# Optimization experiments

Hardware: AMD Instinct MI355X
Metric: run time of the kernel (lower is better)

## Reference

```python
import jax, jax.numpy as jnp
import numpy as np

B, D = 8192, 512
MARGIN, CR_BETA, NUM_CLASSES = 0.2, 0.1, 1000


def setup_inputs() -> dict:
    key = jax.random.key(0)
    k1, k2, k3, k4 = jax.random.split(key, 4)
    return {
        "img": jax.random.normal(k1, (B, D), jnp.float32),
        "txt": jax.random.normal(k2, (B, D), jnp.float32),
        "txt_cr": jax.random.normal(k3, (B, D), jnp.float32),
        "labels": jax.random.randint(k4, (B,), 0, NUM_CLASSES),
        "auto_margin_flag": 1,
        "margin": jnp.full((B,), MARGIN, jnp.float32),  # opt.margin repeated per row
        "cr_beta": CR_BETA,
    }


def _similarity(a, b):
    # row-normalize then full cosine-similarity matrix + matched (diagonal) sims
    an = a / (jnp.linalg.norm(a, axis=1, keepdims=True) + 1e-8)
    bn = b / (jnp.linalg.norm(b, axis=1, keepdims=True) + 1e-8)
    return an @ bn.T, jnp.sum(an * bn, axis=1)


def _dir_loss(sim, labels, margin, auto_flag):
    # semi-hard negative mining per anchor row, fully vectorized.
    # Deterministic stand-in for np.random.choice: first valid negative index.
    diag = jnp.diagonal(sim)                               # sim[idx, idx]
    neg_mask = labels[None, :] != labels[:, None]          # [B,B] negatives
    loss_mat = sim - diag[:, None] + margin[:, None]       # triplet margin term
    valid = neg_mask & (loss_mat > 0) & (loss_mat < margin[:, None])
    valid = jax.lax.stop_gradient(valid)                   # mining is detached (numpy in torch)
    has_valid = jnp.any(valid, axis=1)
    if auto_flag:
        row_ok = (margin >= 0.16) & has_valid
    else:
        row_ok = has_valid
    neg_idx = jnp.argmax(valid, axis=1)                    # first valid negative
    sim_an = jnp.take_along_axis(sim, neg_idx[:, None], axis=1)[:, 0]
    per_row = jax.nn.relu(margin - diag + sim_an)
    return jnp.sum(jnp.where(row_ok, per_row, 0.0))


def _cr_loss(img, txt, txt_cr, labels, auto_flag, margin, cr_beta):
    sim, sm = _similarity(img, txt)
    sim_cr, sm_cr = _similarity(img, txt_cr)
    if auto_flag:
        lam = jnp.abs(jax.lax.stop_gradient(sm_cr)) / jnp.abs(jax.lax.stop_gradient(sm))
        lam = jnp.minimum(lam, 1.0)                        # clamp lambda_cr to <= 1
        margin_cr = (lam + 1.0) * margin / 2.0
    else:
        margin_cr = margin / 2.0
    margin_cr = jax.lax.stop_gradient(margin_cr)
    base = _dir_loss(sim, labels, margin, auto_flag) + _dir_loss(sim.T, labels, margin, auto_flag)
    cr = _dir_loss(sim_cr, labels, margin_cr, auto_flag) + _dir_loss(sim_cr.T, labels, margin_cr, auto_flag)
    return base + cr_beta * cr


def reference(img, txt, txt_cr, labels, auto_margin_flag, margin, cr_beta):
    return _cr_loss(img, txt, txt_cr, labels, bool(auto_margin_flag), margin, cr_beta)
```

## Files before the change

kernel.cpp:

```cpp
#include <hip/hip_runtime.h>
#include <climits>

#define NB 8192
#define ND 512

#define WCHUNKS 16
#define WMAXT 4
#define TCHUNKS ((NB - 64) / 64)


__global__ __launch_bounds__(256) void stats_k(
        const float* __restrict__ img, const float* __restrict__ txt,
        const float* __restrict__ cr, const float* __restrict__ margin,
        const int* __restrict__ flagp,
        float* rnImg, float* rnTxt, float* rnCr,
        float* dgSim, float* dgCr, float* mgCr,
        int* negIdx, int* stragCnt, float* out) {
    int tid = threadIdx.x, bid = blockIdx.x;
    int g = bid * 256 + tid;
    if (g < 4 * NB) negIdx[g] = INT_MAX;
    if (bid == 0 && tid < 8) stragCnt[tid] = 0;
    if (bid == 0 && tid == 0) out[0] = 0.0f;

    int r = bid * 16 + (tid >> 4);
    int q = tid & 15;
    const float4* iv = (const float4*)(img + (size_t)r * ND);
    const float4* tv = (const float4*)(txt + (size_t)r * ND);
    const float4* cv = (const float4*)(cr  + (size_t)r * ND);
    float sii = 0, stt = 0, scc = 0, sit = 0, sic = 0;
    #pragma unroll
    for (int i = 0; i < 8; ++i) {
        int k = q + i * 16;
        float4 x = iv[k], y = tv[k], w = cv[k];
        sii += x.x*x.x + x.y*x.y + x.z*x.z + x.w*x.w;
        stt += y.x*y.x + y.y*y.y + y.z*y.z + y.w*y.w;
        scc += w.x*w.x + w.y*w.y + w.z*w.z + w.w*w.w;
        sit += x.x*y.x + x.y*y.y + x.z*y.z + x.w*y.w;
        sic += x.x*w.x + x.y*w.y + x.z*w.z + x.w*w.w;
    }
    #pragma unroll
    for (int off = 1; off < 16; off <<= 1) {
        sii += __shfl_xor(sii, off); stt += __shfl_xor(stt, off);
        scc += __shfl_xor(scc, off); sit += __shfl_xor(sit, off);
        sic += __shfl_xor(sic, off);
    }
    if (q == 0) {
        float rnI = 1.0f / (sqrtf(sii) + 1e-8f);
        float rnT = 1.0f / (sqrtf(stt) + 1e-8f);
        float rnC = 1.0f / (sqrtf(scc) + 1e-8f);
        float ds = sit * rnI * rnT;
        float dc = sic * rnI * rnC;
        float m  = margin[r];
        float mcr = flagp[0] ? (fminf(fabsf(dc) / fabsf(ds), 1.0f) + 1.0f) * m * 0.5f
                             : m * 0.5f;
        rnImg[r] = rnI; rnTxt[r] = rnT; rnCr[r] = rnC;
        dgSim[r] = ds;  dgCr[r]  = dc;  mgCr[r] = mcr;
    }
}

__device__ inline void pass_arrays(int z,
        const float* img, const float* txt, const float* cr,
        const float* rnImg, const float* rnTxt, const float* rnCr,
        const float* dgSim, const float* dgCr,
        const float* margin, const float* mgCr,
        const float*& A, const float*& B, const float*& rnA, const float*& rnB,
        const float*& dgA, const float*& mgA) {
    if (z == 0)      { A = img; B = txt; rnA = rnImg; rnB = rnTxt; dgA = dgSim; mgA = margin; }
    else if (z == 1) { A = txt; B = img; rnA = rnTxt; rnB = rnImg; dgA = dgSim; mgA = margin; }
    else if (z == 2) { A = img; B = cr;  rnA = rnImg; rnB = rnCr;  dgA = dgCr;  mgA = mgCr;   }
    else             { A = cr;  B = img; rnA = rnCr;  rnB = rnImg; dgA = dgCr;  mgA = mgCr;   }
}

__global__ __launch_bounds__(256) void band_k(
        const float* __restrict__ img, const float* __restrict__ txt,
        const float* __restrict__ cr, const int* __restrict__ labels,
        const int* __restrict__ flagp, const float* __restrict__ margin,
        const float* __restrict__ betap,
        const float* rnImg, const float* rnTxt, const float* rnCr,
        const float* dgSim, const float* dgCr, const float* mgCr,
        int* stragCnt, int* stragList, float* out) {
    __shared__ __align__(16) float As[16][64];
    __shared__ __align__(16) float Bs[16][64];
    __shared__ float aRn[64], aDg[64], aMg[64], colRn[64];
    __shared__ int   aLab[64], colLab[64], resIdx[64];
    __shared__ float blockAcc;

    const int tid = threadIdx.x, z = blockIdx.y, a0 = blockIdx.x * 64;
    const int flag = flagp[0];
    const float *A, *B, *rnA, *rnB, *dgA, *mgA;
    pass_arrays(z, img, txt, cr, rnImg, rnTxt, rnCr, dgSim, dgCr, margin, mgCr,
                A, B, rnA, rnB, dgA, mgA);

    if (tid < 64) {
        int a = a0 + tid;
        float mg = mgA[a];
        aRn[tid] = rnA[a]; aDg[tid] = dgA[a]; aMg[tid] = mg;
        aLab[tid] = labels[a];
        colRn[tid] = rnB[tid]; colLab[tid] = labels[tid];
        resIdx[tid] = (flag && mg < 0.16f) ? -1 : INT_MAX;
    }
    if (tid == 0) blockAcc = 0.0f;

    const int ty4  = (tid >> 4) * 4, tx4 = (tid & 15) * 4;
    const int lrow = tid >> 2,  lk4 = (tid & 3) * 4;

    float acc[4][4];
    #pragma unroll
    for (int i = 0; i < 4; ++i)
        #pragma unroll
        for (int j = 0; j < 4; ++j) acc[i][j] = 0.0f;

    float4 va = *(const float4*)(A + (size_t)(a0 + lrow) * ND + lk4);
    float4 vb = *(const float4*)(B + (size_t)lrow * ND + lk4);
    for (int kc = 0; kc < ND; kc += 16) {
        __syncthreads();
        As[lk4 + 0][lrow] = va.x; As[lk4 + 1][lrow] = va.y;
        As[lk4 + 2][lrow] = va.z; As[lk4 + 3][lrow] = va.w;
        Bs[lk4 + 0][lrow] = vb.x; Bs[lk4 + 1][lrow] = vb.y;
        Bs[lk4 + 2][lrow] = vb.z; Bs[lk4 + 3][lrow] = vb.w;
        if (kc + 16 < ND) {
            va = *(const float4*)(A + (size_t)(a0 + lrow) * ND + kc + 16 + lk4);
            vb = *(const float4*)(B + (size_t)lrow * ND + kc + 16 + lk4);
        }
        __syncthreads();
        #pragma unroll
        for (int k = 0; k < 16; ++k) {
            float4 av = *(const float4*)&As[k][ty4];
            float4 bv = *(const float4*)&Bs[k][tx4];
            float ar[4] = {av.x, av.y, av.z, av.w};
            float br[4] = {bv.x, bv.y, bv.z, bv.w};
            #pragma unroll
            for (int i = 0; i < 4; ++i)
                #pragma unroll
                for (int j = 0; j < 4; ++j)
                    acc[i][j] = fmaf(ar[i], br[j], acc[i][j]);
        }
    }
    __syncthreads();

    #pragma unroll
    for (int i = 0; i < 4; ++i) {
        int r = ty4 + i;
        float mgv = aMg[r];
        if (flag && mgv < 0.16f) continue;
        float dg = aDg[r], rna = aRn[r];
        int la = aLab[r];
        #pragma unroll
        for (int j = 0; j < 4; ++j) {
            int c = tx4 + j;
            if (colLab[c] == la) continue;
            float v  = acc[i][j] * rna * colRn[c];
            float lm = v - dg + mgv;
            if (lm > 0.0f && lm < mgv) atomicMin(&resIdx[r], c);
        }
    }
    __syncthreads();

    #pragma unroll
    for (int i = 0; i < 4; ++i) {
        int r = ty4 + i;
        int w = resIdx[r];
        if (w < 0 || w == INT_MAX) continue;
        int c = w - tx4;
        if (c < 0 || c > 3) continue;
        float v  = acc[i][c] * aRn[r] * colRn[w];
        float lm = v - aDg[r] + aMg[r];
        atomicAdd(&blockAcc, lm);
    }
    __syncthreads();

    if (tid < 64 && resIdx[tid] == INT_MAX) {
        int pos = atomicAdd(&stragCnt[z], 1);
        stragList[z * NB + pos] = a0 + tid;
    }
    if (tid == 0 && blockAcc != 0.0f) {
        float scale = (z >= 2) ? betap[0] : 1.0f;
        atomicAdd(out, blockAcc * scale);
    }
}

__global__ __launch_bounds__(256) void wina_k(
        const float* __restrict__ img, const float* __restrict__ txt,
        const float* __restrict__ cr, const int* __restrict__ labels,
        const float* __restrict__ margin,
        const float* rnImg, const float* rnTxt, const float* rnCr,
        const float* dgSim, const float* dgCr, const float* mgCr,
        const int* stragCnt, const int* stragList, int* negIdx) {
    __shared__ __align__(16) float As[16][64];
    __shared__ __align__(16) float Bs[16][64];
    __shared__ float aRn[64], aDg[64], aMg[64], colRn[64];
    __shared__ int   aId[64], aRowS[64], aLab[64], colLab[64];

    const int tid = threadIdx.x, z = blockIdx.y;
    const int chunk = blockIdx.x & (WCHUNKS - 1);
    const int t     = blockIdx.x / WCHUNKS;
    const int cnt = stragCnt[z];
    if (t * 64 >= cnt) return;
    const int c0 = 64 + chunk * 64;

    const float *A, *B, *rnA, *rnB, *dgA, *mgA;
    pass_arrays(z, img, txt, cr, rnImg, rnTxt, rnCr, dgSim, dgCr, margin, mgCr,
                A, B, rnA, rnB, dgA, mgA);

    if (tid < 64) {
        int s = t * 64 + tid;
        int a = (s < cnt) ? stragList[z * NB + s] : -1;
        int ar = (a >= 0) ? a : 0;
        aId[tid] = a; aRowS[tid] = ar;
        aRn[tid] = rnA[ar]; aDg[tid] = dgA[ar]; aMg[tid] = mgA[ar];
        aLab[tid] = labels[ar];
        colRn[tid] = rnB[c0 + tid]; colLab[tid] = labels[c0 + tid];
    }
    __syncthreads();

    const int ty4  = (tid >> 4) * 4, tx4 = (tid & 15) * 4;
    const int lrow = tid >> 2,  lk4 = (tid & 3) * 4;

    float acc[4][4];
    #pragma unroll
    for (int i = 0; i < 4; ++i)
        #pragma unroll
        for (int j = 0; j < 4; ++j) acc[i][j] = 0.0f;

    float4 va = *(const float4*)(A + (size_t)aRowS[lrow] * ND + lk4);
    float4 vb = *(const float4*)(B + (size_t)(c0 + lrow) * ND + lk4);
    for (int kc = 0; kc < ND; kc += 16) {
        __syncthreads();
        As[lk4 + 0][lrow] = va.x; As[lk4 + 1][lrow] = va.y;
        As[lk4 + 2][lrow] = va.z; As[lk4 + 3][lrow] = va.w;
        Bs[lk4 + 0][lrow] = vb.x; Bs[lk4 + 1][lrow] = vb.y;
        Bs[lk4 + 2][lrow] = vb.z; Bs[lk4 + 3][lrow] = vb.w;
        if (kc + 16 < ND) {
            va = *(const float4*)(A + (size_t)aRowS[lrow] * ND + kc + 16 + lk4);
            vb = *(const float4*)(B + (size_t)(c0 + lrow) * ND + kc + 16 + lk4);
        }
        __syncthreads();
        #pragma unroll
        for (int k = 0; k < 16; ++k) {
            float4 av = *(const float4*)&As[k][ty4];
            float4 bv = *(const float4*)&Bs[k][tx4];
            float ar[4] = {av.x, av.y, av.z, av.w};
            float br[4] = {bv.x, bv.y, bv.z, bv.w};
            #pragma unroll
            for (int i = 0; i < 4; ++i)
                #pragma unroll
                for (int j = 0; j < 4; ++j)
                    acc[i][j] = fmaf(ar[i], br[j], acc[i][j]);
        }
    }
    __syncthreads();

    #pragma unroll
    for (int i = 0; i < 4; ++i) {
        int r = ty4 + i;
        int a = aId[r];
        if (a < 0) continue;
        float dg = aDg[r], mgv = aMg[r], rna = aRn[r];
        int la = aLab[r];
        #pragma unroll
        for (int j = 0; j < 4; ++j) {
            int c = tx4 + j;
            if (colLab[c] == la) continue;
            float lm = acc[i][j] * rna * colRn[c] - dg + mgv;
            if (lm > 0.0f && lm < mgv) atomicMin(&negIdx[z * NB + a], c0 + c);
        }
    }
}

__global__ __launch_bounds__(256) void tail_k(
        const float* __restrict__ img, const float* __restrict__ txt,
        const float* __restrict__ cr, const int* __restrict__ labels,
        const float* __restrict__ margin,
        const float* rnImg, const float* rnTxt, const float* rnCr,
        const float* dgSim, const float* dgCr, const float* mgCr,
        const int* stragCnt, const int* stragList, int* negIdx) {
    __shared__ __align__(16) float As[16][64];
    __shared__ __align__(16) float Bs[16][64];
    __shared__ float aRn[64], aDg[64], aMg[64], colRn[64];
    __shared__ int   aId[64], aRowS[64], aLab[64], colLab[64];
    __shared__ int   sSurv[512];
    __shared__ int   sNa;

    const int tid = threadIdx.x, z = blockIdx.y;
    const int c0 = 64 + blockIdx.x * 64;
    const int cnt = stragCnt[z];
    if (cnt == 0) return;

    const float *A, *B, *rnA, *rnB, *dgA, *mgA;
    pass_arrays(z, img, txt, cr, rnImg, rnTxt, rnCr, dgSim, dgCr, margin, mgCr,
                A, B, rnA, rnB, dgA, mgA);

    if (tid == 0) sNa = 0;
    __syncthreads();
    for (int s = tid; s < cnt; s += 256) {
        int a = stragList[z * NB + s];
        if (negIdx[z * NB + a] == INT_MAX) {
            int p = atomicAdd(&sNa, 1);
            if (p < 512) sSurv[p] = a;
        }
    }
    __syncthreads();
    const int na = min(sNa, 512);
    if (na == 0) return;

    if (tid < 64) { colRn[tid] = rnB[c0 + tid]; colLab[tid] = labels[c0 + tid]; }

    const int ty4  = (tid >> 4) * 4, tx4 = (tid & 15) * 4;
    const int lrow = tid >> 2,  lk4 = (tid & 3) * 4;

    for (int s0 = 0; s0 < na; s0 += 64) {
        __syncthreads();
        if (tid < 64) {
            int s = s0 + tid;
            int a = (s < na) ? sSurv[s] : -1;
            int ar = (a >= 0) ? a : 0;
            aId[tid] = a; aRowS[tid] = ar;
            aRn[tid] = rnA[ar]; aDg[tid] = dgA[ar]; aMg[tid] = mgA[ar];
            aLab[tid] = labels[ar];
        }
        __syncthreads();

        float acc[4][4];
        #pragma unroll
        for (int i = 0; i < 4; ++i)
            #pragma unroll
            for (int j = 0; j < 4; ++j) acc[i][j] = 0.0f;

        float4 va = *(const float4*)(A + (size_t)aRowS[lrow] * ND + lk4);
        float4 vb = *(const float4*)(B + (size_t)(c0 + lrow) * ND + lk4);
        for (int kc = 0; kc < ND; kc += 16) {
            __syncthreads();
            As[lk4 + 0][lrow] = va.x; As[lk4 + 1][lrow] = va.y;
            As[lk4 + 2][lrow] = va.z; As[lk4 + 3][lrow] = va.w;
            Bs[lk4 + 0][lrow] = vb.x; Bs[lk4 + 1][lrow] = vb.y;
            Bs[lk4 + 2][lrow] = vb.z; Bs[lk4 + 3][lrow] = vb.w;
            if (kc + 16 < ND) {
                va = *(const float4*)(A + (size_t)aRowS[lrow] * ND + kc + 16 + lk4);
                vb = *(const float4*)(B + (size_t)(c0 + lrow) * ND + kc + 16 + lk4);
            }
            __syncthreads();
            #pragma unroll
            for (int k = 0; k < 16; ++k) {
                float4 av = *(const float4*)&As[k][ty4];
                float4 bv = *(const float4*)&Bs[k][tx4];
                float ar[4] = {av.x, av.y, av.z, av.w};
                float br[4] = {bv.x, bv.y, bv.z, bv.w};
                #pragma unroll
                for (int i = 0; i < 4; ++i)
                    #pragma unroll
                    for (int j = 0; j < 4; ++j)
                        acc[i][j] = fmaf(ar[i], br[j], acc[i][j]);
            }
        }
        __syncthreads();

        #pragma unroll
        for (int i = 0; i < 4; ++i) {
            int r = ty4 + i;
            int a = aId[r];
            if (a < 0) continue;
            float dg = aDg[r], mgv = aMg[r], rna = aRn[r];
            int la = aLab[r];
            #pragma unroll
            for (int j = 0; j < 4; ++j) {
                int c = tx4 + j;
                if (colLab[c] == la) continue;
                float lm = acc[i][j] * rna * colRn[c] - dg + mgv;
                if (lm > 0.0f && lm < mgv) atomicMin(&negIdx[z * NB + a], c0 + c);
            }
        }
    }
}

__global__ __launch_bounds__(256) void final_k(
        const float* __restrict__ img, const float* __restrict__ txt,
        const float* __restrict__ cr,
        const float* rnImg, const float* rnTxt, const float* rnCr,
        const float* dgSim, const float* dgCr,
        const float* __restrict__ margin, const float* mgCr,
        const float* __restrict__ betap,
        const int* stragCnt, const int* stragList, const int* negIdx,
        float* out) {
    __shared__ float s4[4];
    const int tid = threadIdx.x, z = blockIdx.y;
    const float *A, *B, *rnA, *rnB, *dgA, *mgA;
    pass_arrays(z, img, txt, cr, rnImg, rnTxt, rnCr, dgSim, dgCr, margin, mgCr,
                A, B, rnA, rnB, dgA, mgA);
    int t = blockIdx.x * 256 + tid;
    float contrib = 0.0f;
    if (t < stragCnt[z]) {
        int a = stragList[z * NB + t];
        int idx = negIdx[z * NB + a];
        if (idx != INT_MAX) {
            const float4* Av = (const float4*)(A + (size_t)a   * ND);
            const float4* Bv = (const float4*)(B + (size_t)idx * ND);
            float d = 0.0f;
            #pragma unroll 8
            for (int i = 0; i < ND / 4; ++i) {
                float4 x = Av[i], y = Bv[i];
                d += x.x*y.x + x.y*y.y + x.z*y.z + x.w*y.w;
            }
            float lm = d * rnA[a] * rnB[idx] - dgA[a] + mgA[a];
            contrib = fmaxf(lm, 0.0f);
        }
    }
    #pragma unroll
    for (int off = 32; off; off >>= 1) contrib += __shfl_xor(contrib, off);
    if ((tid & 63) == 0) s4[tid >> 6] = contrib;
    __syncthreads();
    if (tid == 0) {
        float sum = s4[0] + s4[1] + s4[2] + s4[3];
        if (sum != 0.0f) atomicAdd(out, sum * ((z >= 2) ? betap[0] : 1.0f));
    }
}


__global__ __launch_bounds__(256) void zero_k(float* out, int n) {
    int g = blockIdx.x * 256 + threadIdx.x;
    if (g < n) out[g] = 0.0f;
}

template <int U>
__device__ void stragScan(const float* __restrict__ A, const float* __restrict__ B,
                          const int* __restrict__ labels, int a0, int u, int scol,
                          const int* sList, int g0,
                          const float* aRn, const float* aDg, const float* aMg,
                          const int* aLab, int* sMin8, int* doneMask,
                          float* blockAcc) {
    const int tid = threadIdx.x;
    float rn_s[U], dg_s[U], mg_s[U];
    int lab_s[U];
    const float4* Av[U];
    #pragma unroll
    for (int s = 0; s < U; ++s) {
        int slot = sList[g0 + (s < u ? s : 0)];
        rn_s[s] = aRn[slot]; dg_s[s] = aDg[slot]; mg_s[s] = aMg[slot];
        lab_s[s] = aLab[slot];
        Av[s] = (const float4*)(A + (size_t)(a0 + slot) * ND);
    }
    if (tid < U) sMin8[tid] = INT_MAX;
    if (tid == 0) *doneMask = 0;
    __syncthreads();
    for (int jb = scol; jb < NB; jb += 256) {
        int j = jb + tid;
        bool jv = (j < NB);
        int mask = *doneMask;
        float dot[U];
        #pragma unroll
        for (int s = 0; s < U; ++s) dot[s] = 0.0f;
        float ssq = 0.0f;
        if (jv) {
            const float4* Bv = (const float4*)(B + (size_t)j * ND);
            #pragma unroll 4
            for (int k4 = 0; k4 < ND / 4; ++k4) {
                float4 b = Bv[k4];
                ssq += b.x*b.x + b.y*b.y + b.z*b.z + b.w*b.w;
                #pragma unroll
                for (int s = 0; s < U; ++s) {
                    float4 a = Av[s][k4];
                    dot[s] += a.x*b.x + a.y*b.y + a.z*b.z + a.w*b.w;
                }
            }
        }
        float rnb = 1.0f / (sqrtf(ssq) + 1e-8f);
        int lj = jv ? labels[j] : -1;
        float lmv[U];
        #pragma unroll
        for (int s = 0; s < U; ++s) {
            lmv[s] = dot[s] * rn_s[s] * rnb - dg_s[s] + mg_s[s];
            if (jv && s < u && !((mask >> s) & 1) && lj != lab_s[s] &&
                lmv[s] > 0.0f && lmv[s] < mg_s[s])
                atomicMin(&sMin8[s], j);
        }
        __syncthreads();
        #pragma unroll
        for (int s = 0; s < U; ++s)
            if (jv && s < u && !((mask >> s) & 1) && sMin8[s] == j)
                atomicAdd(blockAcc, lmv[s]);
        __syncthreads();
        if (tid == 0) {
            int m2 = 0;
            for (int s = 0; s < u; ++s)
                if (sMin8[s] != INT_MAX) m2 |= (1 << s);
            *doneMask = m2;
        }
        __syncthreads();
        if (*doneMask == (1 << u) - 1) break;
    }
}

__global__ __launch_bounds__(256) void mine_k(const float* __restrict__ img,
                                              const float* __restrict__ txt,
                                              const float* __restrict__ cr,
                                              const int*   __restrict__ labels,
                                              const int*   __restrict__ flagp,
                                              const float* __restrict__ margin,
                                              const float* __restrict__ betap,
                                              float* __restrict__ out) {
    __shared__ __align__(16) float As[16][64];
    __shared__ __align__(16) float Bs[16][64];
    __shared__ float aRn[64], aDg[64], aMg[64];
    __shared__ int   aLab[64];
    __shared__ float colRn[64];
    __shared__ int   colLab[64];
    __shared__ int   resIdx[64], prevIdx[64];
    __shared__ int   cnt;
    __shared__ float blockAcc;
    __shared__ int   sList[64];
    __shared__ int   sCnt;
    __shared__ int   sMin8[8];
    __shared__ int   doneMask;

    const int tid  = threadIdx.x;
    const int z    = blockIdx.y;
    const int a0   = blockIdx.x * 64;
    const int flag = flagp[0];
    const float* A = (z == 1) ? txt : (z == 3) ? cr : img;
    const float* B = (z == 0) ? txt : (z == 2) ? cr : img;
    {
        int ar = tid >> 2, q = tid & 3;
        int a  = a0 + ar;
        const float4* iv = (const float4*)(img + (size_t)a * ND) + q * 32;
        const float4* tv = (const float4*)(txt + (size_t)a * ND) + q * 32;
        const float4* cv = (const float4*)(cr  + (size_t)a * ND) + q * 32;
        float sii = 0, stt = 0, scc = 0, sit = 0, sic = 0;
        #pragma unroll 4
        for (int i = 0; i < 32; ++i) {
            float4 x = iv[i], y = tv[i], w = cv[i];
            sii += x.x*x.x + x.y*x.y + x.z*x.z + x.w*x.w;
            stt += y.x*y.x + y.y*y.y + y.z*y.z + y.w*y.w;
            scc += w.x*w.x + w.y*w.y + w.z*w.z + w.w*w.w;
            sit += x.x*y.x + x.y*y.y + x.z*y.z + x.w*y.w;
            sic += x.x*w.x + x.y*w.y + x.z*w.z + x.w*w.w;
        }
        sii += __shfl_xor(sii, 1); sii += __shfl_xor(sii, 2);
        stt += __shfl_xor(stt, 1); stt += __shfl_xor(stt, 2);
        sit += __shfl_xor(sit, 1); sit += __shfl_xor(sit, 2);
        scc += __shfl_xor(scc, 1); scc += __shfl_xor(scc, 2);
        sic += __shfl_xor(sic, 1); sic += __shfl_xor(sic, 2);
        if (q == 0) {
            float rnI = 1.0f / (sqrtf(sii) + 1e-8f);
            float rnT = 1.0f / (sqrtf(stt) + 1e-8f);
            float ds  = sit * rnI * rnT;
            float m   = margin[a];
            float mg, rna, dgv;
            if (z >= 2) {
                float rnC = 1.0f / (sqrtf(scc) + 1e-8f);
                float dc  = sic * rnI * rnC;
                mg = flag ? (fminf(fabsf(dc) / fabsf(ds), 1.0f) + 1.0f) * m * 0.5f
                          : m * 0.5f;
                dgv = dc; rna = (z == 3) ? rnC : rnI;
            } else {
                mg = m; dgv = ds; rna = (z == 1) ? rnT : rnI;
            }
            aRn[ar] = rna; aDg[ar] = dgv; aMg[ar] = mg; aLab[ar] = labels[a];
            resIdx[ar] = (flag && mg < 0.16f) ? -1 : INT_MAX;
        }
        if (tid == 0) blockAcc = 0.0f;
    }
    __syncthreads();
    const int ty4  = (tid >> 4) * 4, tx4 = (tid & 15) * 4;
    const int lrow = tid >> 2,  lk4 = (tid & 3) * 4;
    int bandCols = 0, unresolved = 64;
    for (int jc = 0; jc < 2; ++jc) {
        int j0 = jc * 64;
        float acc[4][4];
        #pragma unroll
        for (int i = 0; i < 4; ++i)
            #pragma unroll
            for (int j = 0; j < 4; ++j) acc[i][j] = 0.0f;
        float bssq = 0.0f;
        for (int kc = 0; kc < ND; kc += 16) {
            __syncthreads();
            float4 va = *(const float4*)(A + (size_t)(a0 + lrow) * ND + kc + lk4);
            float4 vb = *(const float4*)(B + (size_t)(j0 + lrow) * ND + kc + lk4);
            As[lk4 + 0][lrow] = va.x; As[lk4 + 1][lrow] = va.y;
            As[lk4 + 2][lrow] = va.z; As[lk4 + 3][lrow] = va.w;
            Bs[lk4 + 0][lrow] = vb.x; Bs[lk4 + 1][lrow] = vb.y;
            Bs[lk4 + 2][lrow] = vb.z; Bs[lk4 + 3][lrow] = vb.w;
            bssq += vb.x*vb.x + vb.y*vb.y + vb.z*vb.z + vb.w*vb.w;
            __syncthreads();
            #pragma unroll
            for (int k = 0; k < 16; ++k) {
                float4 av = *(const float4*)&As[k][ty4];
                float4 bv = *(const float4*)&Bs[k][tx4];
                float ar[4] = {av.x, av.y, av.z, av.w};
                float br[4] = {bv.x, bv.y, bv.z, bv.w};
                #pragma unroll
                for (int i = 0; i < 4; ++i)
                    #pragma unroll
                    for (int j = 0; j < 4; ++j)
                        acc[i][j] = fmaf(ar[i], br[j], acc[i][j]);
            }
        }
        bssq += __shfl_xor(bssq, 1); bssq += __shfl_xor(bssq, 2);
        __syncthreads();
        if ((tid & 3) == 0) {
            colRn[lrow]  = 1.0f / (sqrtf(bssq) + 1e-8f);
            colLab[lrow] = labels[j0 + lrow];
        }
        if (tid < 64) prevIdx[tid] = resIdx[tid];
        __syncthreads();
        #pragma unroll
        for (int i = 0; i < 4; ++i) {
            int r = ty4 + i;
            if (prevIdx[r] != INT_MAX) continue;
            float dg = aDg[r], mgv = aMg[r], rna = aRn[r];
            int la = aLab[r];
            #pragma unroll
            for (int j = 0; j < 4; ++j) {
                int c = tx4 + j;
                if (colLab[c] == la) continue;
                float v  = acc[i][j] * rna * colRn[c];
                float lm = v - dg + mgv;
                if (lm > 0.0f && lm < mgv) atomicMin(&resIdx[r], j0 + c);
            }
        }
        __syncthreads();
        #pragma unroll
        for (int i = 0; i < 4; ++i) {
            int r = ty4 + i;
            if (prevIdx[r] != INT_MAX) continue;
            int w = resIdx[r];
            if (w == INT_MAX) continue;
            int c = w - j0 - tx4;
            if (c < 0 || c > 3) continue;
            float v  = acc[i][c] * aRn[r] * colRn[tx4 + c];
            float lm = v - aDg[r] + aMg[r];
            atomicAdd(&blockAcc, lm);
        }
        __syncthreads();
        if (tid == 0) cnt = 0;
        __syncthreads();
        if (tid < 64 && resIdx[tid] == INT_MAX) atomicAdd(&cnt, 1);
        __syncthreads();
        unresolved = cnt;
        bandCols = j0 + 64;
        __syncthreads();
        if (unresolved <= 8) break;
    }
    if (unresolved > 0) {
        if (tid == 0) sCnt = 0;
        __syncthreads();
        if (tid < 64 && resIdx[tid] == INT_MAX) {
            int pos = atomicAdd(&sCnt, 1);
            sList[pos] = tid;
        }
        __syncthreads();
        int total = sCnt;
        for (int g0 = 0; g0 < total; g0 += 8) {
            int u = min(8, total - g0);
            if (u == 1)      stragScan<1>(A, B, labels, a0, u, bandCols, sList, g0, aRn, aDg, aMg, aLab, sMin8, &doneMask, &blockAcc);
            else if (u == 2) stragScan<2>(A, B, labels, a0, u, bandCols, sList, g0, aRn, aDg, aMg, aLab, sMin8, &doneMask, &blockAcc);
            else if (u <= 4) stragScan<4>(A, B, labels, a0, u, bandCols, sList, g0, aRn, aDg, aMg, aLab, sMin8, &doneMask, &blockAcc);
            else             stragScan<8>(A, B, labels, a0, u, bandCols, sList, g0, aRn, aDg, aMg, aLab, sMin8, &doneMask, &blockAcc);
            __syncthreads();
        }
    }
    if (tid == 0 && blockAcc != 0.0f) {
        float scale = (z >= 2) ? betap[0] : 1.0f;
        atomicAdd(out, blockAcc * scale);
    }
}


extern "C" void kernel_launch(void* const* d_in, const int* in_sizes, int n_in,
                              void* d_out, int out_size, void* d_ws, size_t ws_size,
                              hipStream_t stream) {
    const float* img    = (const float*)d_in[0];
    const float* txt    = (const float*)d_in[1];
    const float* cr     = (const float*)d_in[2];
    const int*   labels = (const int*)  d_in[3];
    const int*   flagp  = (const int*)  d_in[4];
    const float* marg   = (const float*)d_in[5];
    const float* betap  = (const float*)d_in[6];
    float* out = (float*)d_out;
    (void)in_sizes; (void)n_in;

    const size_t REQ = (size_t)(6 * NB) * 4 + (size_t)(4 * NB) * 4 + 64 +
                       (size_t)(4 * NB) * 4;
    if (ws_size >= REQ) {
        float* wf = (float*)d_ws;
        float* rnImg = wf + 0 * NB;
        float* rnTxt = wf + 1 * NB;
        float* rnCr  = wf + 2 * NB;
        float* dgSim = wf + 3 * NB;
        float* dgCr  = wf + 4 * NB;
        float* mgCr  = wf + 5 * NB;
        int* negIdx    = (int*)(wf + 6 * NB);
        int* stragCnt  = negIdx + 4 * NB;
        int* stragList = stragCnt + 16;

        stats_k<<<dim3(NB / 16),              dim3(256), 0, stream>>>(
            img, txt, cr, marg, flagp,
            rnImg, rnTxt, rnCr, dgSim, dgCr, mgCr, negIdx, stragCnt, out);
        band_k <<<dim3(NB / 64, 4),           dim3(256), 0, stream>>>(
            img, txt, cr, labels, flagp, marg, betap,
            rnImg, rnTxt, rnCr, dgSim, dgCr, mgCr, stragCnt, stragList, out);
        wina_k <<<dim3(WCHUNKS * WMAXT, 4),   dim3(256), 0, stream>>>(
            img, txt, cr, labels, marg,
            rnImg, rnTxt, rnCr, dgSim, dgCr, mgCr,
            stragCnt, stragList, negIdx);
        tail_k <<<dim3(TCHUNKS, 4),           dim3(256), 0, stream>>>(
            img, txt, cr, labels, marg,
            rnImg, rnTxt, rnCr, dgSim, dgCr, mgCr,
            stragCnt, stragList, negIdx);
        final_k<<<dim3(NB / 256, 4),          dim3(256), 0, stream>>>(
            img, txt, cr, rnImg, rnTxt, rnCr, dgSim, dgCr, marg, mgCr, betap,
            stragCnt, stragList, negIdx, out);
    } else {
        zero_k<<<dim3((out_size + 255) / 256), dim3(256), 0, stream>>>(out, out_size);
        mine_k<<<dim3(NB / 64, 4), dim3(256), 0, stream>>>(img, txt, cr, labels,
                                                           flagp, marg, betap, out);
    }
}
```

Before: 229.1 us.

## Shrink band/window GEMM tiles to 32x64 and rewrite tail as wave-per-column dot products

Band and window kernels now use a shared 32x64 GEMM helper with padded shared-memory tiles, doubling block count to improve occupancy and load balance across CUs. The tail kernel replaces the 64x64 tiled GEMM with loading 8 surviving anchor rows into LDS and computing dot products per wave with shuffle reductions, which avoids wasting a full tile when only a few stragglers remain. The tail survivor cap drops from 512 to 256 per chunk, which could change results if more stragglers survive.

```diff
diff --git a/kernel.cpp b/kernel.cpp
--- a/kernel.cpp
+++ b/kernel.cpp
@@ -5,7 +5,7 @@
 #define ND 512
 
 #define WCHUNKS 16
-#define WMAXT 4
+#define WTILES 8
 #define TCHUNKS ((NB - 64) / 64)
 
 
@@ -71,6 +71,48 @@
     else             { A = cr;  B = img; rnA = rnCr;  rnB = rnImg; dgA = dgCr;  mgA = mgCr;   }
 }
 
+template <bool GATHER>
+__device__ __forceinline__ void gemm32x64(
+        const float* __restrict__ A, const float* __restrict__ B,
+        int a0, const int* aRow, int c0,
+        float (&As)[16][36], float (&Bs)[16][68],
+        float (&acc)[2][4], int tid) {
+    const int ty2 = (tid >> 4) * 2, tx4 = (tid & 15) * 4;
+    const int lrow = tid >> 2, lk4 = (tid & 3) * 4;
+    const bool doA = tid < 128;
+    const int arow = GATHER ? (doA ? aRow[lrow] : 0) : (a0 + (lrow & 31));
+    float4 va, vb;
+    if (doA) va = *(const float4*)(A + (size_t)arow * ND + lk4);
+    vb = *(const float4*)(B + (size_t)(c0 + lrow) * ND + lk4);
+    for (int kc = 0; kc < ND; kc += 16) {
+        __syncthreads();
+        if (doA) {
+            As[lk4 + 0][lrow] = va.x; As[lk4 + 1][lrow] = va.y;
+            As[lk4 + 2][lrow] = va.z; As[lk4 + 3][lrow] = va.w;
+        }
+        Bs[lk4 + 0][lrow] = vb.x; Bs[lk4 + 1][lrow] = vb.y;
+        Bs[lk4 + 2][lrow] = vb.z; Bs[lk4 + 3][lrow] = vb.w;
+        if (kc + 16 < ND) {
+            if (doA) va = *(const float4*)(A + (size_t)arow * ND + kc + 16 + lk4);
+            vb = *(const float4*)(B + (size_t)(c0 + lrow) * ND + kc + 16 + lk4);
+        }
+        __syncthreads();
+        #pragma unroll
+        for (int k = 0; k < 16; ++k) {
+            float2 av = *(const float2*)&As[k][ty2];
+            float4 bv = *(const float4*)&Bs[k][tx4];
+            #pragma unroll
+            for (int i = 0; i < 2; ++i) {
+                float ai = i ? av.y : av.x;
+                acc[i][0] = fmaf(ai, bv.x, acc[i][0]);
+                acc[i][1] = fmaf(ai, bv.y, acc[i][1]);
+                acc[i][2] = fmaf(ai, bv.z, acc[i][2]);
+                acc[i][3] = fmaf(ai, bv.w, acc[i][3]);
+            }
+        }
+    }
+}
+
 __global__ __launch_bounds__(256) void band_k(
         const float* __restrict__ img, const float* __restrict__ txt,
         const float* __restrict__ cr, const int* __restrict__ labels,
@@ -79,68 +121,37 @@
         const float* rnImg, const float* rnTxt, const float* rnCr,
         const float* dgSim, const float* dgCr, const float* mgCr,
         int* stragCnt, int* stragList, float* out) {
-    __shared__ __align__(16) float As[16][64];
-    __shared__ __align__(16) float Bs[16][64];
-    __shared__ float aRn[64], aDg[64], aMg[64], colRn[64];
-    __shared__ int   aLab[64], colLab[64], resIdx[64];
+    __shared__ __align__(16) float As[16][36];
+    __shared__ __align__(16) float Bs[16][68];
+    __shared__ float aRn[32], aDg[32], aMg[32], colRn[64];
+    __shared__ int   aLab[32], colLab[64], resIdx[32];
     __shared__ float blockAcc;
 
-    const int tid = threadIdx.x, z = blockIdx.y, a0 = blockIdx.x * 64;
+    const int tid = threadIdx.x, z = blockIdx.y, a0 = blockIdx.x * 32;
     const int flag = flagp[0];
     const float *A, *B, *rnA, *rnB, *dgA, *mgA;
     pass_arrays(z, img, txt, cr, rnImg, rnTxt, rnCr, dgSim, dgCr, margin, mgCr,
                 A, B, rnA, rnB, dgA, mgA);
 
-    if (tid < 64) {
+    if (tid < 32) {
         int a = a0 + tid;
         float mg = mgA[a];
         aRn[tid] = rnA[a]; aDg[tid] = dgA[a]; aMg[tid] = mg;
         aLab[tid] = labels[a];
-        colRn[tid] = rnB[tid]; colLab[tid] = labels[tid];
         resIdx[tid] = (flag && mg < 0.16f) ? -1 : INT_MAX;
     }
+    if (tid < 64) { colRn[tid] = rnB[tid]; colLab[tid] = labels[tid]; }
     if (tid == 0) blockAcc = 0.0f;
-
-    const int ty4  = (tid >> 4) * 4, tx4 = (tid & 15) * 4;
-    const int lrow = tid >> 2,  lk4 = (tid & 3) * 4;
-
-    float acc[4][4];
+    __syncthreads();
+
+    float acc[2][4] = {};
+    gemm32x64<false>(A, B, a0, nullptr, 0, As, Bs, acc, tid);
+    __syncthreads();
+
+    const int ty2 = (tid >> 4) * 2, tx4 = (tid & 15) * 4;
     #pragma unroll
-    for (int i = 0; i < 4; ++i)
-        #pragma unroll
-        for (int j = 0; j < 4; ++j) acc[i][j] = 0.0f;
-
-    float4 va = *(const float4*)(A + (size_t)(a0 + lrow) * ND + lk4);
-    float4 vb = *(const float4*)(B + (size_t)lrow * ND + lk4);
-    for (int kc = 0; kc < ND; kc += 16) {
-        __syncthreads();
-        As[lk4 + 0][lrow] = va.x; As[lk4 + 1][lrow] = va.y;
-        As[lk4 + 2][lrow] = va.z; As[lk4 + 3][lrow] = va.w;
-        Bs[lk4 + 0][lrow] = vb.x; Bs[lk4 + 1][lrow] = vb.y;
-        Bs[lk4 + 2][lrow] = vb.z; Bs[lk4 + 3][lrow] = vb.w;
-        if (kc + 16 < ND) {
-            va = *(const float4*)(A + (size_t)(a0 + lrow) * ND + kc + 16 + lk4);
-            vb = *(const float4*)(B + (size_t)lrow * ND + kc + 16 + lk4);
-        }
-        __syncthreads();
-        #pragma unroll
-        for (int k = 0; k < 16; ++k) {
-            float4 av = *(const float4*)&As[k][ty4];
-            float4 bv = *(const float4*)&Bs[k][tx4];
-            float ar[4] = {av.x, av.y, av.z, av.w};
-            float br[4] = {bv.x, bv.y, bv.z, bv.w};
-            #pragma unroll
-            for (int i = 0; i < 4; ++i)
-                #pragma unroll
-                for (int j = 0; j < 4; ++j)
-                    acc[i][j] = fmaf(ar[i], br[j], acc[i][j]);
-        }
-    }
-    __syncthreads();
-
-    #pragma unroll
-    for (int i = 0; i < 4; ++i) {
-        int r = ty4 + i;
+    for (int i = 0; i < 2; ++i) {
+        int r = ty2 + i;
         float mgv = aMg[r];
         if (flag && mgv < 0.16f) continue;
         float dg = aDg[r], rna = aRn[r];
@@ -149,27 +160,25 @@
         for (int j = 0; j < 4; ++j) {
             int c = tx4 + j;
             if (colLab[c] == la) continue;
-            float v  = acc[i][j] * rna * colRn[c];
-            float lm = v - dg + mgv;
+            float lm = acc[i][j] * rna * colRn[c] - dg + mgv;
             if (lm > 0.0f && lm < mgv) atomicMin(&resIdx[r], c);
         }
     }
     __syncthreads();
 
     #pragma unroll
-    for (int i = 0; i < 4; ++i) {
-        int r = ty4 + i;
+    for (int i = 0; i < 2; ++i) {
+        int r = ty2 + i;
         int w = resIdx[r];
         if (w < 0 || w == INT_MAX) continue;
         int c = w - tx4;
         if (c < 0 || c > 3) continue;
-        float v  = acc[i][c] * aRn[r] * colRn[w];
-        float lm = v - aDg[r] + aMg[r];
+        float lm = acc[i][c] * aRn[r] * colRn[w] - aDg[r] + aMg[r];
         atomicAdd(&blockAcc, lm);
     }
     __syncthreads();
 
-    if (tid < 64 && resIdx[tid] == INT_MAX) {
+    if (tid < 32 && resIdx[tid] == INT_MAX) {
         int pos = atomicAdd(&stragCnt[z], 1);
         stragList[z * NB + pos] = a0 + tid;
     }
@@ -186,73 +195,41 @@
         const float* rnImg, const float* rnTxt, const float* rnCr,
         const float* dgSim, const float* dgCr, const float* mgCr,
         const int* stragCnt, const int* stragList, int* negIdx) {
-    __shared__ __align__(16) float As[16][64];
-    __shared__ __align__(16) float Bs[16][64];
-    __shared__ float aRn[64], aDg[64], aMg[64], colRn[64];
-    __shared__ int   aId[64], aRowS[64], aLab[64], colLab[64];
+    __shared__ __align__(16) float As[16][36];
+    __shared__ __align__(16) float Bs[16][68];
+    __shared__ float aRn[32], aDg[32], aMg[32], colRn[64];
+    __shared__ int   aId[32], aRow[32], aLab[32], colLab[64];
 
     const int tid = threadIdx.x, z = blockIdx.y;
     const int chunk = blockIdx.x & (WCHUNKS - 1);
     const int t     = blockIdx.x / WCHUNKS;
     const int cnt = stragCnt[z];
-    if (t * 64 >= cnt) return;
+    if (t * 32 >= cnt) return;
     const int c0 = 64 + chunk * 64;
 
     const float *A, *B, *rnA, *rnB, *dgA, *mgA;
     pass_arrays(z, img, txt, cr, rnImg, rnTxt, rnCr, dgSim, dgCr, margin, mgCr,
                 A, B, rnA, rnB, dgA, mgA);
 
-    if (tid < 64) {
-        int s = t * 64 + tid;
+    if (tid < 32) {
+        int s = t * 32 + tid;
         int a = (s < cnt) ? stragList[z * NB + s] : -1;
         int ar = (a >= 0) ? a : 0;
-        aId[tid] = a; aRowS[tid] = ar;
+        aId[tid] = a; aRow[tid] = ar;
         aRn[tid] = rnA[ar]; aDg[tid] = dgA[ar]; aMg[tid] = mgA[ar];
         aLab[tid] = labels[ar];
-        colRn[tid] = rnB[c0 + tid]; colLab[tid] = labels[c0 + tid];
-    }
-    __syncthreads();
-
-    const int ty4  = (tid >> 4) * 4, tx4 = (tid & 15) * 4;
-    const int lrow = tid >> 2,  lk4 = (tid & 3) * 4;
-
-    float acc[4][4];
+    }
+    if (tid < 64) { colRn[tid] = rnB[c0 + tid]; colLab[tid] = labels[c0 + tid]; }
+    __syncthreads();
+
+    float acc[2][4] = {};
+    gemm32x64<true>(A, B, 0, aRow, c0, As, Bs, acc, tid);
+    __syncthreads();
+
+    const int ty2 = (tid >> 4) * 2, tx4 = (tid & 15) * 4;
     #pragma unroll
-    for (int i = 0; i < 4; ++i)
-        #pragma unroll
-        for (int j = 0; j < 4; ++j) acc[i][j] = 0.0f;
-
-    float4 va = *(const float4*)(A + (size_t)aRowS[lrow] * ND + lk4);
-    float4 vb = *(const float4*)(B + (size_t)(c0 + lrow) * ND + lk4);
-    for (int kc = 0; kc < ND; kc += 16) {
-        __syncthreads();
-        As[lk4 + 0][lrow] = va.x; As[lk4 + 1][lrow] = va.y;
-        As[lk4 + 2][lrow] = va.z; As[lk4 + 3][lrow] = va.w;
-        Bs[lk4 + 0][lrow] = vb.x; Bs[lk4 + 1][lrow] = vb.y;
-        Bs[lk4 + 2][lrow] = vb.z; Bs[lk4 + 3][lrow] = vb.w;
-        if (kc + 16 < ND) {
-            va = *(const float4*)(A + (size_t)aRowS[lrow] * ND + kc + 16 + lk4);
-            vb = *(const float4*)(B + (size_t)(c0 + lrow) * ND + kc + 16 + lk4);
-        }
-        __syncthreads();
-        #pragma unroll
-        for (int k = 0; k < 16; ++k) {
-            float4 av = *(const float4*)&As[k][ty4];
-            float4 bv = *(const float4*)&Bs[k][tx4];
-            float ar[4] = {av.x, av.y, av.z, av.w};
-            float br[4] = {bv.x, bv.y, bv.z, bv.w};
-            #pragma unroll
-            for (int i = 0; i < 4; ++i)
-                #pragma unroll
-                for (int j = 0; j < 4; ++j)
-                    acc[i][j] = fmaf(ar[i], br[j], acc[i][j]);
-        }
-    }
-    __syncthreads();
-
-    #pragma unroll
-    for (int i = 0; i < 4; ++i) {
-        int r = ty4 + i;
+    for (int i = 0; i < 2; ++i) {
+        int r = ty2 + i;
         int a = aId[r];
         if (a < 0) continue;
         float dg = aDg[r], mgv = aMg[r], rna = aRn[r];
@@ -265,6 +242,12 @@
             if (lm > 0.0f && lm < mgv) atomicMin(&negIdx[z * NB + a], c0 + c);
         }
     }
+}
+
+__device__ inline float dot8(const float4& a0, const float4& a1,
+                             const float4& b0, const float4& b1) {
+    return a0.x*b0.x + a0.y*b0.y + a0.z*b0.z + a0.w*b0.w
+         + a1.x*b1.x + a1.y*b1.y + a1.z*b1.z + a1.w*b1.w;
 }
 
 __global__ __launch_bounds__(256) void tail_k(
@@ -274,11 +257,12 @@
         const float* rnImg, const float* rnTxt, const float* rnCr,
         const float* dgSim, const float* dgCr, const float* mgCr,
         const int* stragCnt, const int* stragList, int* negIdx) {
-    __shared__ __align__(16) float As[16][64];
-    __shared__ __align__(16) float Bs[16][64];
-    __shared__ float aRn[64], aDg[64], aMg[64], colRn[64];
-    __shared__ int   aId[64], aRowS[64], aLab[64], colLab[64];
-    __shared__ int   sSurv[512];
+    __shared__ __align__(16) float Aload[8][ND];
+    __shared__ float sRn[8], sDg[8], sMg[8];
+    __shared__ int   sLab[8], sAid[8];
+    __shared__ float colRn_s[64];
+    __shared__ int   colLab_s[64];
+    __shared__ int   sSurv[256];
     __shared__ int   sNa;
 
     const int tid = threadIdx.x, z = blockIdx.y;
@@ -296,77 +280,75 @@
         int a = stragList[z * NB + s];
         if (negIdx[z * NB + a] == INT_MAX) {
             int p = atomicAdd(&sNa, 1);
-            if (p < 512) sSurv[p] = a;
-        }
-    }
-    __syncthreads();
-    const int na = min(sNa, 512);
+            if (p < 256) sSurv[p] = a;
+        }
+    }
+    __syncthreads();
+    const int na = min(sNa, 256);
     if (na == 0) return;
 
-    if (tid < 64) { colRn[tid] = rnB[c0 + tid]; colLab[tid] = labels[c0 + tid]; }
-
-    const int ty4  = (tid >> 4) * 4, tx4 = (tid & 15) * 4;
-    const int lrow = tid >> 2,  lk4 = (tid & 3) * 4;
-
-    for (int s0 = 0; s0 < na; s0 += 64) {
-        __syncthreads();
-        if (tid < 64) {
-            int s = s0 + tid;
-            int a = (s < na) ? sSurv[s] : -1;
-            int ar = (a >= 0) ? a : 0;
-            aId[tid] = a; aRowS[tid] = ar;
-            aRn[tid] = rnA[ar]; aDg[tid] = dgA[ar]; aMg[tid] = mgA[ar];
-            aLab[tid] = labels[ar];
-        }
-        __syncthreads();
-
-        float acc[4][4];
-        #pragma unroll
-        for (int i = 0; i < 4; ++i)
+    if (tid < 64) { colRn_s[tid] = rnB[c0 + tid]; colLab_s[tid] = labels[c0 + tid]; }
+
+    const int wv = tid >> 6, lane = tid & 63;
+
+    for (int g0 = 0; g0 < na; g0 += 8) {
+        const int gn = min(8, na - g0);
+        __syncthreads();
+        if (tid < 8) {
+            int s = g0 + ((tid < gn) ? tid : 0);
+            int a = sSurv[s];
+            sAid[tid] = (tid < gn) ? a : -1;
+            sRn[tid] = rnA[a]; sDg[tid] = dgA[a]; sMg[tid] = mgA[a];
+            sLab[tid] = labels[a];
+        }
+        #pragma unroll
+        for (int m = 0; m < 4; ++m) {
+            int idx = tid + m * 256;
+            int row = idx >> 7, f4 = idx & 127;
+            int a = sSurv[g0 + ((row < gn) ? row : 0)];
+            *(float4*)&Aload[row][f4 * 4] =
+                *(const float4*)(A + (size_t)a * ND + f4 * 4);
+        }
+        __syncthreads();
+
+        for (int cb = 0; cb < 16; cb += 4) {
+            const int cc0 = wv * 16 + cb;
+            float4 b0[4], b1[4];
             #pragma unroll
-            for (int j = 0; j < 4; ++j) acc[i][j] = 0.0f;
-
-        float4 va = *(const float4*)(A + (size_t)aRowS[lrow] * ND + lk4);
-        float4 vb = *(const float4*)(B + (size_t)(c0 + lrow) * ND + lk4);
-        for (int kc = 0; kc < ND; kc += 16) {
-            __syncthreads();
-            As[lk4 + 0][lrow] = va.x; As[lk4 + 1][lrow] = va.y;
-            As[lk4 + 2][lrow] = va.z; As[lk4 + 3][lrow] = va.w;
-            Bs[lk4 + 0][lrow] = vb.x; Bs[lk4 + 1][lrow] = vb.y;
-            Bs[lk4 + 2][lrow] = vb.z; Bs[lk4 + 3][lrow] = vb.w;
-            if (kc + 16 < ND) {
-                va = *(const float4*)(A + (size_t)aRowS[lrow] * ND + kc + 16 + lk4);
-                vb = *(const float4*)(B + (size_t)(c0 + lrow) * ND + kc + 16 + lk4);
-            }
-            __syncthreads();
+            for (int q = 0; q < 4; ++q) {
+                const float4* Bv = (const float4*)(B + (size_t)(c0 + cc0 + q) * ND);
+                b0[q] = Bv[lane]; b1[q] = Bv[lane + 64];
+            }
             #pragma unroll
-            for (int k = 0; k < 16; ++k) {
-                float4 av = *(const float4*)&As[k][ty4];
-                float4 bv = *(const float4*)&Bs[k][tx4];
-                float ar[4] = {av.x, av.y, av.z, av.w};
-                float br[4] = {bv.x, bv.y, bv.z, bv.w};
+            for (int s = 0; s < 8; ++s) {
+                float4 a0v = *(const float4*)&Aload[s][lane * 4];
+                float4 a1v = *(const float4*)&Aload[s][(lane + 64) * 4];
+                float d0 = dot8(a0v, a1v, b0[0], b1[0]);
+                float d1 = dot8(a0v, a1v, b0[1], b1[1]);
+                float d2 = dot8(a0v, a1v, b0[2], b1[2]);
+                float d3 = dot8(a0v, a1v, b0[3], b1[3]);
                 #pragma unroll
-                for (int i = 0; i < 4; ++i)
-                    #pragma unroll
-                    for (int j = 0; j < 4; ++j)
-                        acc[i][j] = fmaf(ar[i], br[j], acc[i][j]);
-            }
-        }
-        __syncthreads();
-
-        #pragma unroll
-        for (int i = 0; i < 4; ++i) {
-            int r = ty4 + i;
-            int a = aId[r];
-            if (a < 0) continue;
-            float dg = aDg[r], mgv = aMg[r], rna = aRn[r];
-            int la = aLab[r];
-            #pragma unroll
-            for (int j = 0; j < 4; ++j) {
-                int c = tx4 + j;
-                if (colLab[c] == la) continue;
-                float lm = acc[i][j] * rna * colRn[c] - dg + mgv;
-                if (lm > 0.0f && lm < mgv) atomicMin(&negIdx[z * NB + a], c0 + c);
+                for (int off = 1; off < 64; off <<= 1) {
+                    d0 += __shfl_xor(d0, off); d1 += __shfl_xor(d1, off);
+                    d2 += __shfl_xor(d2, off); d3 += __shfl_xor(d3, off);
+                }
+                if (lane == 0) {
+                    int aid = sAid[s];
+                    if (aid >= 0) {
+                        float rn = sRn[s], dg = sDg[s], mg = sMg[s];
+                        int lb = sLab[s];
+                        float dv[4] = {d0, d1, d2, d3};
+                        #pragma unroll
+                        for (int q = 0; q < 4; ++q) {
+                            int cc = cc0 + q;
+                            if (colLab_s[cc] != lb) {
+                                float lm = dv[q] * rn * colRn_s[cc] - dg + mg;
+                                if (lm > 0.0f && lm < mg)
+                                    atomicMin(&negIdx[z * NB + aid], c0 + cc);
+                            }
+                        }
+                    }
+                }
             }
         }
     }
@@ -694,10 +676,10 @@
         stats_k<<<dim3(NB / 16),              dim3(256), 0, stream>>>(
             img, txt, cr, marg, flagp,
             rnImg, rnTxt, rnCr, dgSim, dgCr, mgCr, negIdx, stragCnt, out);
-        band_k <<<dim3(NB / 64, 4),           dim3(256), 0, stream>>>(
+        band_k <<<dim3(NB / 32, 4),           dim3(256), 0, stream>>>(
             img, txt, cr, labels, flagp, marg, betap,
             rnImg, rnTxt, rnCr, dgSim, dgCr, mgCr, stragCnt, stragList, out);
-        wina_k <<<dim3(WCHUNKS * WMAXT, 4),   dim3(256), 0, stream>>>(
+        wina_k <<<dim3(WCHUNKS * WTILES, 4),  dim3(256), 0, stream>>>(
             img, txt, cr, labels, marg,
             rnImg, rnTxt, rnCr, dgSim, dgCr, mgCr,
             stragCnt, stragList, negIdx);
```

Result: slower. 242.1 us (+5.7%).
